# Kernel optimization log

Measured on AMD Instinct MI355X. Metric: run time of the kernel, lower is better.

The kernel has to match this reference:

```python
import jax, jax.numpy as jnp
import numpy as np

B, T, D, H = 128, 1024, 48, 256  # batch, seq_len, input_dim, hidden_dim


def _lstm_dir(x, valid, Wih, Whh, bih, bhh, reverse):
    """One direction of one LSTM layer over padded batch.
    x: [B,T,F], valid: [B,T] bool (t < length). Returns (outs [B,T,H], h_final [B,H]).
    Emulates pack_padded_sequence semantics: state frozen (fwd) / held at zero (bwd)
    outside valid range, outputs zeroed at padded steps."""
    Bn = x.shape[0]
    Hn = Whh.shape[1]
    xs = (jnp.swapaxes(x, 0, 1), valid.T)  # time-major
    init = (jnp.zeros((Bn, Hn), x.dtype), jnp.zeros((Bn, Hn), x.dtype))

    def step(carry, inp):
        h, c = carry
        xt, vt = inp
        gates = xt @ Wih.T + bih + h @ Whh.T + bhh  # [B,4H], PyTorch i,f,g,o order
        i, f, g, o = jnp.split(gates, 4, axis=-1)
        i = jax.nn.sigmoid(i)
        f = jax.nn.sigmoid(f)
        g = jnp.tanh(g)
        o = jax.nn.sigmoid(o)
        c_new = f * c + i * g
        h_new = o * jnp.tanh(c_new)
        m = vt[:, None]
        return (jnp.where(m, h_new, h), jnp.where(m, c_new, c)), jnp.where(m, h_new, 0.0)

    (hT, _), outs = jax.lax.scan(step, init, xs, reverse=reverse)
    return jnp.swapaxes(outs, 0, 1), hT


def setup_inputs() -> dict:
    key = jax.random.key(0)
    ks = jax.random.split(key, 32)
    k_lstm = 1.0 / np.sqrt(H)
    u = lambda k, shape, bound: jax.random.uniform(k, shape, jnp.float32, -bound, bound)
    inp = {
        "x": jax.random.normal(ks[0], (B, T, D), jnp.float32),
        "lengths": jax.random.randint(ks[1], (B,), 1, T + 1, jnp.int64 if jax.config.jax_enable_x64 else jnp.int32).astype(jnp.int32),
    }
    # layer 0 (input D), layer 1 (input 2H); fwd and bwd directions
    inp["w_ih_l0f"] = u(ks[2], (4 * H, D), k_lstm)
    inp["w_hh_l0f"] = u(ks[3], (4 * H, H), k_lstm)
    inp["b_ih_l0f"] = u(ks[4], (4 * H,), k_lstm)
    inp["b_hh_l0f"] = u(ks[5], (4 * H,), k_lstm)
    inp["w_ih_l0b"] = u(ks[6], (4 * H, D), k_lstm)
    inp["w_hh_l0b"] = u(ks[7], (4 * H, H), k_lstm)
    inp["b_ih_l0b"] = u(ks[8], (4 * H,), k_lstm)
    inp["b_hh_l0b"] = u(ks[9], (4 * H,), k_lstm)
    inp["w_ih_l1f"] = u(ks[10], (4 * H, 2 * H), k_lstm)
    inp["w_hh_l1f"] = u(ks[11], (4 * H, H), k_lstm)
    inp["b_ih_l1f"] = u(ks[12], (4 * H,), k_lstm)
    inp["b_hh_l1f"] = u(ks[13], (4 * H,), k_lstm)
    inp["w_ih_l1b"] = u(ks[14], (4 * H, 2 * H), k_lstm)
    inp["w_hh_l1b"] = u(ks[15], (4 * H, H), k_lstm)
    inp["b_ih_l1b"] = u(ks[16], (4 * H,), k_lstm)
    inp["b_hh_l1b"] = u(ks[17], (4 * H,), k_lstm)
    # MLP head: fc1 (2H -> H), fc2 (H -> 1)
    k1 = 1.0 / np.sqrt(2 * H)
    k2 = 1.0 / np.sqrt(H)
    inp["fc1_w"] = u(ks[18], (H, 2 * H), k1)
    inp["fc1_b"] = u(ks[19], (H,), k1)
    inp["fc2_w"] = u(ks[20], (1, H), k2)
    inp["fc2_b"] = u(ks[21], (1,), k2)
    return inp


def reference(x, lengths,
              w_ih_l0f, w_hh_l0f, b_ih_l0f, b_hh_l0f,
              w_ih_l0b, w_hh_l0b, b_ih_l0b, b_hh_l0b,
              w_ih_l1f, w_hh_l1f, b_ih_l1f, b_hh_l1f,
              w_ih_l1b, w_hh_l1b, b_ih_l1b, b_hh_l1b,
              fc1_w, fc1_b, fc2_w, fc2_b):
    valid = jnp.arange(x.shape[1])[None, :] < lengths[:, None]  # [B,T]
    # layer 0
    o0f, _ = _lstm_dir(x, valid, w_ih_l0f, w_hh_l0f, b_ih_l0f, b_hh_l0f, reverse=False)
    o0b, _ = _lstm_dir(x, valid, w_ih_l0b, w_hh_l0b, b_ih_l0b, b_hh_l0b, reverse=True)
    x1 = jnp.concatenate([o0f, o0b], axis=-1)  # [B,T,2H]
    # layer 1 (dropout between layers is inference no-op)
    _, h1f = _lstm_dir(x1, valid, w_ih_l1f, w_hh_l1f, b_ih_l1f, b_hh_l1f, reverse=False)
    _, h1b = _lstm_dir(x1, valid, w_ih_l1b, w_hh_l1b, b_ih_l1b, b_hh_l1b, reverse=True)
    hidden = jnp.concatenate([h1f, h1b], axis=-1)  # [B,2H] = h_n[-2],h_n[-1]
    out = jax.nn.relu(hidden @ fc1_w.T + fc1_b)
    return out @ fc2_w.T + fc2_b  # [B,1]
```

## Files before the change

kernel.cpp:

```cpp
#include <hip/hip_runtime.h>

namespace {

constexpr int B = 128;
constexpr int T = 1024;
constexpr int DIN = 48;
constexpr int H = 256;
constexpr int G = 4 * H;
constexpr int NTHREADS = 512;

constexpr size_t BH          = (size_t)B * H;
constexpr size_t WT_FLOATS   = 4 * 256 * 1024 + 2 * 48 * 1024 + 2 * 512 * 1024;
constexpr size_t STATE_FLOATS= 12 * BH;
constexpr size_t O0_ELEMS    = (size_t)B * T * 512;

__device__ __forceinline__ float sigmoidf_(float x) {
    float z = __expf(-fabsf(x));
    float s = 1.0f / (1.0f + z);
    return x >= 0.0f ? s : 1.0f - s;
}
__device__ __forceinline__ float tanhf_(float x) {
    float z = __expf(-2.0f * fabsf(x));
    float tp = (1.0f - z) / (1.0f + z);
    return x >= 0.0f ? tp : -tp;
}
__device__ __forceinline__ float bf2f(unsigned short s) {
    union { unsigned int u; float f; } v; v.u = ((unsigned int)s) << 16; return v.f;
}
__device__ __forceinline__ unsigned short f2bf(float f) {
    union { float f; unsigned int u; } v; v.f = f;
    unsigned int u = v.u;
    return (unsigned short)((u + 0x7FFFu + ((u >> 16) & 1u)) >> 16);
}

__global__ void zero_f(float* __restrict__ p, int n) {
    int i = blockIdx.x * blockDim.x + threadIdx.x;
    if (i < n) p[i] = 0.0f;
}

__global__ void transpose_w(const float* __restrict__ src, float* __restrict__ dst, int K) {
    int idx = blockIdx.x * blockDim.x + threadIdx.x;
    if (idx >= K * 1024) return;
    int r = idx & 1023;
    int k = idx >> 10;
    dst[idx] = src[r * K + k];
}

template<int INP, int XKK, int XSL, int XPB, int KSMAX, bool WRITE_OUT, typename XT, typename OT>
__global__ __launch_bounds__(NTHREADS)
void lstm_step(int s,
               const XT* __restrict__ xin, int xstride,
               const float* __restrict__ wih_t_f, const float* __restrict__ wih_t_b,
               const float* __restrict__ whh_t_f, const float* __restrict__ whh_t_b,
               const float* __restrict__ bih_f,  const float* __restrict__ bhh_f,
               const float* __restrict__ bih_b,  const float* __restrict__ bhh_b,
               const float* __restrict__ h_in,
               float* __restrict__ h_out,
               float* __restrict__ c_st,
               OT* __restrict__ oout,
               const int* __restrict__ lengths)
{
    const int bx  = blockIdx.x;
    const int d   = bx >> 7;
    const int rem = bx & 127;
    const int b0  = (rem >> 3) * 8;
    const int c0  = (rem & 7) * 32;
    const int tid = threadIdx.x;
    const int ks  = tid & 15;
    const int rq  = tid >> 4;

    const int t = d ? (T - 1 - s) : s;

    const float* wih_t = d ? wih_t_b : wih_t_f;
    const float* whh_t = d ? whh_t_b : whh_t_f;
    const float* bih   = d ? bih_b : bih_f;
    const float* bhh   = d ? bhh_b : bhh_f;
    const float* hrow_in  = h_in  + d * (B * H);
    float*       hrow_out = h_out + d * (B * H);
    float*       crow     = c_st  + d * (B * H);

    __shared__ float4 lds_x4[8 * XPB];
    __shared__ float4 lds_h4[8 * 80];
    __shared__ float  lds_g[128 * 9];

    {
        const int nchunk = INP / 4;
        for (int i = tid; i < 8 * nchunk; i += NTHREADS) {
            int b, k4;
            if constexpr (INP == 48) { b = i / 12; k4 = i - b * 12; }
            else                     { b = i >> 7; k4 = i & 127; }
            const XT* src = xin + ((size_t)(b0 + b) * T + t) * xstride + k4 * 4;
            float4 v;
            if constexpr (sizeof(XT) == 4) {
                v = *(const float4*)src;
            } else {
                ushort4 uv = *(const ushort4*)src;
                v = make_float4(bf2f(uv.x), bf2f(uv.y), bf2f(uv.z), bf2f(uv.w));
            }
            int slot;
            if constexpr (INP == 48) slot = b * XPB + k4 * XSL;
            else                     slot = b * XPB + (k4 >> 3) * XSL + (k4 & 7);
            lds_x4[slot] = v;
        }
    }
    for (int i = tid; i < 8 * 64; i += NTHREADS) {
        int b = i >> 6, k4 = i & 63;
        float4 v = *(const float4*)(hrow_in + (b0 + b) * H + k4 * 4);
        lds_h4[b * 80 + (k4 >> 2) * 5 + (k4 & 3)] = v;
    }
    __syncthreads();

    const int rbase = rq * 4;
    const int gate  = rbase >> 5;
    const int chl4  = rbase & 31;
    const int grow0 = gate * 256 + c0 + chl4;

    float acc[4][8];
    #pragma unroll
    for (int i = 0; i < 4; i++)
        #pragma unroll
        for (int b = 0; b < 8; b++) acc[i][b] = 0.0f;

    if (ks < KSMAX) {
        #pragma unroll
        for (int kk = 0; kk < XKK; kk++) {
            float4 xv[8];
            #pragma unroll
            for (int b = 0; b < 8; b++) xv[b] = lds_x4[b * XPB + ks * XSL + kk];
            const int kbase = (ks * XKK + kk) * 4;
            #pragma unroll
            for (int j = 0; j < 4; j++) {
                float4 w4 = *(const float4*)(wih_t + (kbase + j) * G + grow0);
                #pragma unroll
                for (int b = 0; b < 8; b++) {
                    float xs = (j == 0) ? xv[b].x : (j == 1) ? xv[b].y : (j == 2) ? xv[b].z : xv[b].w;
                    acc[0][b] = fmaf(w4.x, xs, acc[0][b]);
                    acc[1][b] = fmaf(w4.y, xs, acc[1][b]);
                    acc[2][b] = fmaf(w4.z, xs, acc[2][b]);
                    acc[3][b] = fmaf(w4.w, xs, acc[3][b]);
                }
            }
        }
    }

    #pragma unroll
    for (int kk = 0; kk < 4; kk++) {
        float4 hv[8];
        #pragma unroll
        for (int b = 0; b < 8; b++) hv[b] = lds_h4[b * 80 + ks * 5 + kk];
        const int kbase = (ks * 4 + kk) * 4;
        #pragma unroll
        for (int j = 0; j < 4; j++) {
            float4 w4 = *(const float4*)(whh_t + (kbase + j) * G + grow0);
            #pragma unroll
            for (int b = 0; b < 8; b++) {
                float xs = (j == 0) ? hv[b].x : (j == 1) ? hv[b].y : (j == 2) ? hv[b].z : hv[b].w;
                acc[0][b] = fmaf(w4.x, xs, acc[0][b]);
                acc[1][b] = fmaf(w4.y, xs, acc[1][b]);
                acc[2][b] = fmaf(w4.z, xs, acc[2][b]);
                acc[3][b] = fmaf(w4.w, xs, acc[3][b]);
            }
        }
    }

    #pragma unroll
    for (int i = 0; i < 4; i++)
        #pragma unroll
        for (int b = 0; b < 8; b++) {
            float v = acc[i][b];
            v += __shfl_xor(v, 1, 64);
            v += __shfl_xor(v, 2, 64);
            v += __shfl_xor(v, 4, 64);
            v += __shfl_xor(v, 8, 64);
            acc[i][b] = v;
        }
    if (ks == 0) {
        #pragma unroll
        for (int i = 0; i < 4; i++)
            #pragma unroll
            for (int b = 0; b < 8; b++)
                lds_g[(rbase + i) * 9 + b] = acc[i][b];
    }
    __syncthreads();

    if (tid < 256) {
        const int chl = tid & 31;
        const int b   = tid >> 5;
        const int gch = c0 + chl;
        float gi = lds_g[(0 * 32 + chl) * 9 + b] + bih[0 * 256 + gch] + bhh[0 * 256 + gch];
        float gf = lds_g[(1 * 32 + chl) * 9 + b] + bih[1 * 256 + gch] + bhh[1 * 256 + gch];
        float gg = lds_g[(2 * 32 + chl) * 9 + b] + bih[2 * 256 + gch] + bhh[2 * 256 + gch];
        float go = lds_g[(3 * 32 + chl) * 9 + b] + bih[3 * 256 + gch] + bhh[3 * 256 + gch];
        float iv = sigmoidf_(gi);
        float fv = sigmoidf_(gf);
        float gv = tanhf_(gg);
        float ov = sigmoidf_(go);
        const int sidx = (b0 + b) * H + gch;
        float c_old = crow[sidx];
        float h_old = hrow_in[sidx];
        float c_new = fv * c_old + iv * gv;
        float h_new = ov * tanhf_(c_new);
        bool valid = t < lengths[b0 + b];
        if (valid) crow[sidx] = c_new;
        hrow_out[sidx] = valid ? h_new : h_old;
        if constexpr (WRITE_OUT) {
            float hv = valid ? h_new : 0.0f;
            size_t oidx = ((size_t)(b0 + b) * T + t) * 512 + d * 256 + gch;
            if constexpr (sizeof(OT) == 4) oout[oidx] = hv;
            else                           oout[oidx] = f2bf(hv);
        }
    }
}

__global__ __launch_bounds__(256)
void fc_head(const float* __restrict__ h1,
             const float* __restrict__ fc1w, const float* __restrict__ fc1b,
             const float* __restrict__ fc2w, const float* __restrict__ fc2b,
             float* __restrict__ out)
{
    int b = blockIdx.x;
    int tid = threadIdx.x;
    __shared__ float hid[512];
    __shared__ float red[4];
    hid[tid]       = h1[b * H + tid];
    hid[256 + tid] = h1[(size_t)B * H + b * H + tid];
    __syncthreads();
    float a = fc1b[tid];
    const float4* w4 = (const float4*)(fc1w + tid * 512);
    const float4* h4 = (const float4*)hid;
    #pragma unroll 4
    for (int k = 0; k < 128; k++) {
        float4 w = w4[k], h = h4[k];
        a = fmaf(w.x, h.x, a); a = fmaf(w.y, h.y, a);
        a = fmaf(w.z, h.z, a); a = fmaf(w.w, h.w, a);
    }
    float r = fmaxf(a, 0.0f);
    float v = r * fc2w[tid];
    #pragma unroll
    for (int off = 32; off > 0; off >>= 1) v += __shfl_down(v, off, 64);
    if ((tid & 63) == 0) red[tid >> 6] = v;
    __syncthreads();
    if (tid == 0) out[b] = red[0] + red[1] + red[2] + red[3] + fc2b[0];
}

}

extern "C" void kernel_launch(void* const* d_in, const int* in_sizes, int n_in,
                              void* d_out, int out_size, void* d_ws, size_t ws_size,
                              hipStream_t stream)
{
    const float* x        = (const float*)d_in[0];
    const int*   lengths  = (const int*)d_in[1];
    const float* w_ih_l0f = (const float*)d_in[2];
    const float* w_hh_l0f = (const float*)d_in[3];
    const float* b_ih_l0f = (const float*)d_in[4];
    const float* b_hh_l0f = (const float*)d_in[5];
    const float* w_ih_l0b = (const float*)d_in[6];
    const float* w_hh_l0b = (const float*)d_in[7];
    const float* b_ih_l0b = (const float*)d_in[8];
    const float* b_hh_l0b = (const float*)d_in[9];
    const float* w_ih_l1f = (const float*)d_in[10];
    const float* w_hh_l1f = (const float*)d_in[11];
    const float* b_ih_l1f = (const float*)d_in[12];
    const float* b_hh_l1f = (const float*)d_in[13];
    const float* w_ih_l1b = (const float*)d_in[14];
    const float* w_hh_l1b = (const float*)d_in[15];
    const float* b_ih_l1b = (const float*)d_in[16];
    const float* b_hh_l1b = (const float*)d_in[17];
    const float* fc1w     = (const float*)d_in[18];
    const float* fc1b     = (const float*)d_in[19];
    const float* fc2w     = (const float*)d_in[20];
    const float* fc2b     = (const float*)d_in[21];

    float* ws = (float*)d_ws;

    float* whh_t_l0f = ws;
    float* whh_t_l0b = whh_t_l0f + 256 * 1024;
    float* whh_t_l1f = whh_t_l0b + 256 * 1024;
    float* whh_t_l1b = whh_t_l1f + 256 * 1024;
    float* wih_t_l0f = whh_t_l1b + 256 * 1024;
    float* wih_t_l0b = wih_t_l0f + 48 * 1024;
    float* wih_t_l1f = wih_t_l0b + 48 * 1024;
    float* wih_t_l1b = wih_t_l1f + 512 * 1024;

    float* state = ws + WT_FLOATS;
    float* h_l0 = state;
    float* h_l1 = h_l0 + 4 * BH;
    float* c_l0 = h_l1 + 4 * BH;
    float* c_l1 = c_l0 + 2 * BH;
    void*  O0   = (void*)(state + STATE_FLOATS);

    const size_t base_bytes = (WT_FLOATS + STATE_FLOATS) * sizeof(float);
    const bool o0_f32 = ws_size >= base_bytes + O0_ELEMS * sizeof(float);

    zero_f<<<(int)((STATE_FLOATS + 255) / 256), 256, 0, stream>>>(state, (int)STATE_FLOATS);

    transpose_w<<<256 * 1024 / 256, 256, 0, stream>>>(w_hh_l0f, whh_t_l0f, 256);
    transpose_w<<<256 * 1024 / 256, 256, 0, stream>>>(w_hh_l0b, whh_t_l0b, 256);
    transpose_w<<<256 * 1024 / 256, 256, 0, stream>>>(w_hh_l1f, whh_t_l1f, 256);
    transpose_w<<<256 * 1024 / 256, 256, 0, stream>>>(w_hh_l1b, whh_t_l1b, 256);
    transpose_w<<<48 * 1024 / 256, 256, 0, stream>>>(w_ih_l0f, wih_t_l0f, 48);
    transpose_w<<<48 * 1024 / 256, 256, 0, stream>>>(w_ih_l0b, wih_t_l0b, 48);
    transpose_w<<<512 * 1024 / 256, 256, 0, stream>>>(w_ih_l1f, wih_t_l1f, 512);
    transpose_w<<<512 * 1024 / 256, 256, 0, stream>>>(w_ih_l1b, wih_t_l1b, 512);

    if (o0_f32) {
        float* O0f = (float*)O0;
        for (int s = 0; s < T; s++) {
            const float* hin = h_l0 + (size_t)(s & 1) * 2 * BH;
            float* hout      = h_l0 + (size_t)((s & 1) ^ 1) * 2 * BH;
            lstm_step<48, 1, 3, 48, 12, true, float, float><<<256, NTHREADS, 0, stream>>>(
                s, x, DIN,
                wih_t_l0f, wih_t_l0b, whh_t_l0f, whh_t_l0b,
                b_ih_l0f, b_hh_l0f, b_ih_l0b, b_hh_l0b,
                hin, hout, c_l0, O0f, lengths);
        }
        for (int s = 0; s < T; s++) {
            const float* hin = h_l1 + (size_t)(s & 1) * 2 * BH;
            float* hout      = h_l1 + (size_t)((s & 1) ^ 1) * 2 * BH;
            lstm_step<512, 8, 9, 144, 16, false, float, float><<<256, NTHREADS, 0, stream>>>(
                s, O0f, 512,
                wih_t_l1f, wih_t_l1b, whh_t_l1f, whh_t_l1b,
                b_ih_l1f, b_hh_l1f, b_ih_l1b, b_hh_l1b,
                hin, hout, c_l1, (float*)nullptr, lengths);
        }
    } else {
        unsigned short* O0h = (unsigned short*)O0;
        for (int s = 0; s < T; s++) {
            const float* hin = h_l0 + (size_t)(s & 1) * 2 * BH;
            float* hout      = h_l0 + (size_t)((s & 1) ^ 1) * 2 * BH;
            lstm_step<48, 1, 3, 48, 12, true, float, unsigned short><<<256, NTHREADS, 0, stream>>>(
                s, x, DIN,
                wih_t_l0f, wih_t_l0b, whh_t_l0f, whh_t_l0b,
                b_ih_l0f, b_hh_l0f, b_ih_l0b, b_hh_l0b,
                hin, hout, c_l0, O0h, lengths);
        }
        for (int s = 0; s < T; s++) {
            const float* hin = h_l1 + (size_t)(s & 1) * 2 * BH;
            float* hout      = h_l1 + (size_t)((s & 1) ^ 1) * 2 * BH;
            lstm_step<512, 8, 9, 144, 16, false, unsigned short, float><<<256, NTHREADS, 0, stream>>>(
                s, O0h, 512,
                wih_t_l1f, wih_t_l1b, whh_t_l1f, whh_t_l1b,
                b_ih_l1f, b_hh_l1f, b_ih_l1b, b_hh_l1b,
                hin, hout, c_l1, (float*)nullptr, lengths);
        }
    }
    fc_head<<<B, 256, 0, stream>>>(h_l1, fc1w, fc1b, fc2w, fc2b, (float*)d_out);
}
```

Measured before the change: 27.70 ms.

## Replace per-timestep kernel launches with persistent kernel using flag-based group sync

The per-step LSTM launches (2048 of them) are replaced by one persistent kernel of 256 blocks. Each block spins on a per-batch-group atomic counter that its 8 sibling blocks increment after each step, and a grid-wide barrier separates layer 0 from layer 1. The aim is to remove kernel launch and drain overhead on the serial recurrence. In exchange it relies on all 256 blocks being co-resident, and it uses relaxed atomics without explicit release fences, so visibility ordering could be fragile.

```diff
diff --git a/kernel.cpp b/kernel.cpp
--- a/kernel.cpp
+++ b/kernel.cpp
@@ -9,10 +9,11 @@
 constexpr int G = 4 * H;
 constexpr int NTHREADS = 512;
 
-constexpr size_t BH          = (size_t)B * H;
-constexpr size_t WT_FLOATS   = 4 * 256 * 1024 + 2 * 48 * 1024 + 2 * 512 * 1024;
-constexpr size_t STATE_FLOATS= 12 * BH;
-constexpr size_t O0_ELEMS    = (size_t)B * T * 512;
+constexpr size_t BH           = (size_t)B * H;
+constexpr size_t WT_FLOATS    = 4 * 256 * 1024 + 2 * 48 * 1024 + 2 * 512 * 1024;
+constexpr size_t STATE_FLOATS = 12 * BH;
+constexpr size_t FLAG_INTS    = 1024;
+constexpr size_t O0_ELEMS     = (size_t)B * T * 512;
 
 __device__ __forceinline__ float sigmoidf_(float x) {
     float z = __expf(-fabsf(x));
@@ -47,41 +48,20 @@
 }
 
 template<int INP, int XKK, int XSL, int XPB, int KSMAX, bool WRITE_OUT, typename XT, typename OT>
-__global__ __launch_bounds__(NTHREADS)
-void lstm_step(int s,
-               const XT* __restrict__ xin, int xstride,
-               const float* __restrict__ wih_t_f, const float* __restrict__ wih_t_b,
-               const float* __restrict__ whh_t_f, const float* __restrict__ whh_t_b,
-               const float* __restrict__ bih_f,  const float* __restrict__ bhh_f,
-               const float* __restrict__ bih_b,  const float* __restrict__ bhh_b,
-               const float* __restrict__ h_in,
-               float* __restrict__ h_out,
-               float* __restrict__ c_st,
-               OT* __restrict__ oout,
-               const int* __restrict__ lengths)
+__device__ __forceinline__ void step_body(
+    int t, int dsel, int b0, int c0,
+    const XT* __restrict__ xin, int xstride,
+    const float* __restrict__ wih_t, const float* __restrict__ whh_t,
+    const float* __restrict__ bih,  const float* __restrict__ bhh,
+    const float* __restrict__ hrow_in, float* __restrict__ hrow_out,
+    float* __restrict__ crow, OT* __restrict__ oout,
+    const int* __restrict__ lengths,
+    float4* lds_x4, float4* lds_h4, float* lds_g,
+    int* flag_ptr, int wait_target)
 {
-    const int bx  = blockIdx.x;
-    const int d   = bx >> 7;
-    const int rem = bx & 127;
-    const int b0  = (rem >> 3) * 8;
-    const int c0  = (rem & 7) * 32;
     const int tid = threadIdx.x;
     const int ks  = tid & 15;
     const int rq  = tid >> 4;
-
-    const int t = d ? (T - 1 - s) : s;
-
-    const float* wih_t = d ? wih_t_b : wih_t_f;
-    const float* whh_t = d ? whh_t_b : whh_t_f;
-    const float* bih   = d ? bih_b : bih_f;
-    const float* bhh   = d ? bhh_b : bhh_f;
-    const float* hrow_in  = h_in  + d * (B * H);
-    float*       hrow_out = h_out + d * (B * H);
-    float*       crow     = c_st  + d * (B * H);
-
-    __shared__ float4 lds_x4[8 * XPB];
-    __shared__ float4 lds_h4[8 * 80];
-    __shared__ float  lds_g[128 * 9];
 
     {
         const int nchunk = INP / 4;
@@ -103,10 +83,20 @@
             lds_x4[slot] = v;
         }
     }
-    for (int i = tid; i < 8 * 64; i += NTHREADS) {
-        int b = i >> 6, k4 = i & 63;
-        float4 v = *(const float4*)(hrow_in + (b0 + b) * H + k4 * 4);
-        lds_h4[b * 80 + (k4 >> 2) * 5 + (k4 & 3)] = v;
+
+    if (wait_target > 0) {
+        if (tid == 0) {
+            while (__hip_atomic_load(flag_ptr, __ATOMIC_RELAXED, __HIP_MEMORY_SCOPE_AGENT) < wait_target)
+                __builtin_amdgcn_s_sleep(1);
+        }
+        __syncthreads();
+    }
+
+    for (int i = tid; i < 8 * 256; i += NTHREADS) {
+        int b = i >> 8, k = i & 255;
+        float v = __hip_atomic_load(hrow_in + (b0 + b) * H + k,
+                                    __ATOMIC_RELAXED, __HIP_MEMORY_SCOPE_AGENT);
+        ((float*)lds_h4)[(b * 80 + (k >> 4) * 5 + ((k >> 2) & 3)) * 4 + (k & 3)] = v;
     }
     __syncthreads();
 
@@ -197,17 +187,99 @@
         float ov = sigmoidf_(go);
         const int sidx = (b0 + b) * H + gch;
         float c_old = crow[sidx];
-        float h_old = hrow_in[sidx];
+        float h_old = ((float*)lds_h4)[(b * 80 + (gch >> 4) * 5 + ((gch >> 2) & 3)) * 4 + (gch & 3)];
         float c_new = fv * c_old + iv * gv;
         float h_new = ov * tanhf_(c_new);
         bool valid = t < lengths[b0 + b];
         if (valid) crow[sidx] = c_new;
-        hrow_out[sidx] = valid ? h_new : h_old;
+        __hip_atomic_store(hrow_out + sidx, valid ? h_new : h_old,
+                           __ATOMIC_RELAXED, __HIP_MEMORY_SCOPE_AGENT);
         if constexpr (WRITE_OUT) {
             float hv = valid ? h_new : 0.0f;
-            size_t oidx = ((size_t)(b0 + b) * T + t) * 512 + d * 256 + gch;
-            if constexpr (sizeof(OT) == 4) oout[oidx] = hv;
-            else                           oout[oidx] = f2bf(hv);
+            size_t oidx = ((size_t)(b0 + b) * T + t) * 512 + dsel * 256 + gch;
+            if constexpr (sizeof(OT) == 4)
+                __hip_atomic_store(oout + oidx, hv, __ATOMIC_RELAXED, __HIP_MEMORY_SCOPE_AGENT);
+            else
+                __hip_atomic_store(oout + oidx, f2bf(hv), __ATOMIC_RELAXED, __HIP_MEMORY_SCOPE_AGENT);
+        }
+    }
+}
+
+template<typename OT>
+__global__ __launch_bounds__(NTHREADS)
+void lstm_persist(const float* __restrict__ x,
+    const float* __restrict__ wih0f, const float* __restrict__ wih0b,
+    const float* __restrict__ whh0f, const float* __restrict__ whh0b,
+    const float* __restrict__ bih0f, const float* __restrict__ bhh0f,
+    const float* __restrict__ bih0b, const float* __restrict__ bhh0b,
+    const float* __restrict__ wih1f, const float* __restrict__ wih1b,
+    const float* __restrict__ whh1f, const float* __restrict__ whh1b,
+    const float* __restrict__ bih1f, const float* __restrict__ bhh1f,
+    const float* __restrict__ bih1b, const float* __restrict__ bhh1b,
+    float* __restrict__ h_l0, float* __restrict__ h_l1,
+    float* __restrict__ c_l0, float* __restrict__ c_l1,
+    OT* __restrict__ O0, const int* __restrict__ lengths, int* __restrict__ flags)
+{
+    const int bx  = blockIdx.x;
+    const int d   = bx >> 7;
+    const int rem = bx & 127;
+    const int b0  = (rem >> 3) * 8;
+    const int c0  = (rem & 7) * 32;
+    const int tid = threadIdx.x;
+    const int g   = d * 16 + (rem >> 3);
+    int* flag_ptr = &flags[g * 16];
+
+    __shared__ float4 lds_x4[8 * 144];
+    __shared__ float4 lds_h4[8 * 80];
+    __shared__ float  lds_g[128 * 9];
+
+    {
+        const float* wih_t = d ? wih0b : wih0f;
+        const float* whh_t = d ? whh0b : whh0f;
+        const float* bih   = d ? bih0b : bih0f;
+        const float* bhh   = d ? bhh0b : bhh0f;
+        float* crow = c_l0 + d * (B * H);
+        for (int s = 0; s < T; ++s) {
+            const int t = d ? (T - 1 - s) : s;
+            const float* hin = h_l0 + ((size_t)((s & 1) * 2 + d)) * (B * H);
+            float*       hout= h_l0 + ((size_t)(((s & 1) ^ 1) * 2 + d)) * (B * H);
+            step_body<48, 1, 3, 48, 12, true, float, OT>(
+                t, d, b0, c0, x, DIN, wih_t, whh_t, bih, bhh,
+                hin, hout, crow, O0, lengths, lds_x4, lds_h4, lds_g,
+                flag_ptr, 8 * s);
+            __syncthreads();
+            if (tid == 0)
+                __hip_atomic_fetch_add(flag_ptr, 1, __ATOMIC_RELAXED, __HIP_MEMORY_SCOPE_AGENT);
+        }
+    }
+
+    __syncthreads();
+    if (tid == 0) {
+        __threadfence();
+        __hip_atomic_fetch_add(&flags[32 * 16], 1, __ATOMIC_ACQ_REL, __HIP_MEMORY_SCOPE_AGENT);
+        while (__hip_atomic_load(&flags[32 * 16], __ATOMIC_ACQUIRE, __HIP_MEMORY_SCOPE_AGENT) < 256)
+            __builtin_amdgcn_s_sleep(2);
+        __threadfence();
+    }
+    __syncthreads();
+
+    {
+        const float* wih_t = d ? wih1b : wih1f;
+        const float* whh_t = d ? whh1b : whh1f;
+        const float* bih   = d ? bih1b : bih1f;
+        const float* bhh   = d ? bhh1b : bhh1f;
+        float* crow = c_l1 + d * (B * H);
+        for (int s = 0; s < T; ++s) {
+            const int t = d ? (T - 1 - s) : s;
+            const float* hin = h_l1 + ((size_t)((s & 1) * 2 + d)) * (B * H);
+            float*       hout= h_l1 + ((size_t)(((s & 1) ^ 1) * 2 + d)) * (B * H);
+            step_body<512, 8, 9, 144, 16, false, OT, OT>(
+                t, d, b0, c0, O0, 512, wih_t, whh_t, bih, bhh,
+                hin, hout, crow, (OT*)nullptr, lengths, lds_x4, lds_h4, lds_g,
+                flag_ptr, 8 * (T + s));
+            __syncthreads();
+            if (tid == 0)
+                __hip_atomic_fetch_add(flag_ptr, 1, __ATOMIC_RELAXED, __HIP_MEMORY_SCOPE_AGENT);
         }
     }
 }
@@ -288,12 +360,14 @@
     float* h_l1 = h_l0 + 4 * BH;
     float* c_l0 = h_l1 + 4 * BH;
     float* c_l1 = c_l0 + 2 * BH;
-    void*  O0   = (void*)(state + STATE_FLOATS);
-
-    const size_t base_bytes = (WT_FLOATS + STATE_FLOATS) * sizeof(float);
+    int*   flags = (int*)(state + STATE_FLOATS);
+    void*  O0   = (void*)(state + STATE_FLOATS + FLAG_INTS);
+
+    const size_t base_bytes = (WT_FLOATS + STATE_FLOATS + FLAG_INTS) * sizeof(float);
     const bool o0_f32 = ws_size >= base_bytes + O0_ELEMS * sizeof(float);
 
-    zero_f<<<(int)((STATE_FLOATS + 255) / 256), 256, 0, stream>>>(state, (int)STATE_FLOATS);
+    zero_f<<<(int)((STATE_FLOATS + FLAG_INTS + 255) / 256), 256, 0, stream>>>(
+        state, (int)(STATE_FLOATS + FLAG_INTS));
 
     transpose_w<<<256 * 1024 / 256, 256, 0, stream>>>(w_hh_l0f, whh_t_l0f, 256);
     transpose_w<<<256 * 1024 / 256, 256, 0, stream>>>(w_hh_l0b, whh_t_l0b, 256);
@@ -305,45 +379,23 @@
     transpose_w<<<512 * 1024 / 256, 256, 0, stream>>>(w_ih_l1b, wih_t_l1b, 512);
 
     if (o0_f32) {
-        float* O0f = (float*)O0;
-        for (int s = 0; s < T; s++) {
-            const float* hin = h_l0 + (size_t)(s & 1) * 2 * BH;
-            float* hout      = h_l0 + (size_t)((s & 1) ^ 1) * 2 * BH;
-            lstm_step<48, 1, 3, 48, 12, true, float, float><<<256, NTHREADS, 0, stream>>>(
-                s, x, DIN,
-                wih_t_l0f, wih_t_l0b, whh_t_l0f, whh_t_l0b,
-                b_ih_l0f, b_hh_l0f, b_ih_l0b, b_hh_l0b,
-                hin, hout, c_l0, O0f, lengths);
-        }
-        for (int s = 0; s < T; s++) {
-            const float* hin = h_l1 + (size_t)(s & 1) * 2 * BH;
-            float* hout      = h_l1 + (size_t)((s & 1) ^ 1) * 2 * BH;
-            lstm_step<512, 8, 9, 144, 16, false, float, float><<<256, NTHREADS, 0, stream>>>(
-                s, O0f, 512,
-                wih_t_l1f, wih_t_l1b, whh_t_l1f, whh_t_l1b,
-                b_ih_l1f, b_hh_l1f, b_ih_l1b, b_hh_l1b,
-                hin, hout, c_l1, (float*)nullptr, lengths);
-        }
+        lstm_persist<float><<<256, NTHREADS, 0, stream>>>(
+            x,
+            wih_t_l0f, wih_t_l0b, whh_t_l0f, whh_t_l0b,
+            b_ih_l0f, b_hh_l0f, b_ih_l0b, b_hh_l0b,
+            wih_t_l1f, wih_t_l1b, whh_t_l1f, whh_t_l1b,
+            b_ih_l1f, b_hh_l1f, b_ih_l1b, b_hh_l1b,
+            h_l0, h_l1, c_l0, c_l1,
+            (float*)O0, lengths, flags);
     } else {
-        unsigned short* O0h = (unsigned short*)O0;
-        for (int s = 0; s < T; s++) {
-            const float* hin = h_l0 + (size_t)(s & 1) * 2 * BH;
-            float* hout      = h_l0 + (size_t)((s & 1) ^ 1) * 2 * BH;
-            lstm_step<48, 1, 3, 48, 12, true, float, unsigned short><<<256, NTHREADS, 0, stream>>>(
-                s, x, DIN,
-                wih_t_l0f, wih_t_l0b, whh_t_l0f, whh_t_l0b,
-                b_ih_l0f, b_hh_l0f, b_ih_l0b, b_hh_l0b,
-                hin, hout, c_l0, O0h, lengths);
-        }
-        for (int s = 0; s < T; s++) {
-            const float* hin = h_l1 + (size_t)(s & 1) * 2 * BH;
-            float* hout      = h_l1 + (size_t)((s & 1) ^ 1) * 2 * BH;
-            lstm_step<512, 8, 9, 144, 16, false, unsigned short, float><<<256, NTHREADS, 0, stream>>>(
-                s, O0h, 512,
-                wih_t_l1f, wih_t_l1b, whh_t_l1f, whh_t_l1b,
-                b_ih_l1f, b_hh_l1f, b_ih_l1b, b_hh_l1b,
-                hin, hout, c_l1, (float*)nullptr, lengths);
-        }
+        lstm_persist<unsigned short><<<256, NTHREADS, 0, stream>>>(
+            x,
+            wih_t_l0f, wih_t_l0b, whh_t_l0f, whh_t_l0b,
+            b_ih_l0f, b_hh_l0f, b_ih_l0b, b_hh_l0b,
+            wih_t_l1f, wih_t_l1b, whh_t_l1f, whh_t_l1b,
+            b_ih_l1f, b_hh_l1f, b_ih_l1b, b_hh_l1b,
+            h_l0, h_l1, c_l0, c_l1,
+            (unsigned short*)O0, lengths, flags);
     }
     fc_head<<<B, 256, 0, stream>>>(h_l1, fc1w, fc1b, fc2w, fc2b, (float*)d_out);
 }
```

Result: slower. 61.23 ms (+121.0%).
